# Kernel tuning notes

Hardware: AMD Instinct MI355X
Metric: run time of the kernel (lower is better)

The kernel has to match this reference:

```python
import jax, jax.numpy as jnp
import numpy as np

EMB = 1024
HEADS = 16
DH = EMB // HEADS
EPS = 1e-5


def setup_inputs() -> dict:
    key = jax.random.key(0)
    ks = jax.random.split(key, 8)
    s = 0.02
    return {
        "x": jax.random.normal(ks[0], (4, 2048, EMB), dtype=jnp.float32),
        "Wq": jax.random.normal(ks[1], (EMB, EMB), dtype=jnp.float32) * s,
        "Wk": jax.random.normal(ks[2], (EMB, EMB), dtype=jnp.float32) * s,
        "Wv": jax.random.normal(ks[3], (EMB, EMB), dtype=jnp.float32) * s,
        "Wo": jax.random.normal(ks[4], (EMB, EMB), dtype=jnp.float32) * s,
        "bo": jnp.zeros((EMB,), dtype=jnp.float32),
        "W1": jax.random.normal(ks[5], (EMB, 4 * EMB), dtype=jnp.float32) * s,
        "b1": jnp.zeros((4 * EMB,), dtype=jnp.float32),
        "W2": jax.random.normal(ks[6], (4 * EMB, EMB), dtype=jnp.float32) * s,
        "b2": jnp.zeros((EMB,), dtype=jnp.float32),
        "g1": jnp.ones((EMB,), dtype=jnp.float32),
        "beta1": jnp.zeros((EMB,), dtype=jnp.float32),
        "g2": jnp.ones((EMB,), dtype=jnp.float32),
        "beta2": jnp.zeros((EMB,), dtype=jnp.float32),
    }


def _layernorm(x, scale, bias):
    mean = jnp.mean(x, axis=-1, keepdims=True)
    var = jnp.mean((x - mean) ** 2, axis=-1, keepdims=True)  # unbiased=False
    return scale * ((x - mean) / jnp.sqrt(var + EPS)) + bias


def _attention(x, Wq, Wk, Wv, Wo, bo):
    B, S, _ = x.shape
    q = (x @ Wq).reshape(B, S, HEADS, DH).transpose(0, 2, 1, 3)  # b h s d
    k = (x @ Wk).reshape(B, S, HEADS, DH).transpose(0, 2, 1, 3)
    v = (x @ Wv).reshape(B, S, HEADS, DH).transpose(0, 2, 1, 3)
    scores = jnp.einsum("bhqd,bhkd->bhqk", q, k)
    causal = jnp.tril(jnp.ones((S, S), dtype=bool))
    scores = jnp.where(causal, scores, -jnp.inf)
    w = jax.nn.softmax(scores / jnp.sqrt(jnp.float32(DH)), axis=-1)
    ctx = jnp.einsum("bhqk,bhkd->bhqd", w, v).transpose(0, 2, 1, 3).reshape(B, S, HEADS * DH)
    return ctx @ Wo + bo


def reference(x, Wq, Wk, Wv, Wo, bo, W1, b1, W2, b2, g1, beta1, g2, beta2):
    # pre-LN attention + residual
    h = x + _attention(_layernorm(x, g1, beta1), Wq, Wk, Wv, Wo, bo)
    # pre-LN FFN (exact GELU, as torch nn.GELU default) + residual
    y = _layernorm(h, g2, beta2)
    y = jax.nn.gelu(y @ W1 + b1, approximate=False) @ W2 + b2
    return h + y
```

## Files before the change

### kernel.cpp

```cpp
#include <hip/hip_runtime.h>
#include <hip/hip_bf16.h>

#define EMB 1024
#define SEQ 2048
#define BATCH 4
#define TOK (BATCH*SEQ)
#define NH 16
#define DH 64
#define FF 4096

typedef unsigned short u16;
typedef __bf16 bf16x8 __attribute__((ext_vector_type(8)));
typedef float f32x4 __attribute__((ext_vector_type(4)));

union frag_u { uint4 u4; bf16x8 bf; u16 us[8]; };

__device__ __forceinline__ u16 f2bf(float f) {
  union { float f; unsigned u; } a; a.f = f;
  unsigned r = a.u + 0x7fffu + ((a.u >> 16) & 1u);
  return (u16)(r >> 16);
}
__device__ __forceinline__ float bf2f(u16 u) {
  union { unsigned u; float f; } a; a.u = ((unsigned)u) << 16; return a.f;
}

__device__ __forceinline__ void glds16(const void* g, void* l) {
  __builtin_amdgcn_global_load_lds((const __attribute__((address_space(1))) void*)g,
                                   (__attribute__((address_space(3))) void*)l, 16, 0, 0);
}

__device__ __forceinline__ float gelu_fast(float u) {
  float u2 = u * u;
  float c = fmaf(u2, 0.0356774081f, 0.7978845608f);
  float e = __expf(2.f * u * c);
  return u * e * __builtin_amdgcn_rcpf(e + 1.f);
}

__device__ __forceinline__ void cvt_t_body(const float* __restrict__ src,
                                           u16* __restrict__ dst,
                                           int N, int ldk, int bx, int by) {
  __shared__ float tile[32][33];
  int c0 = bx * 32, r0 = by * 32;
  int tc = threadIdx.x & 31, tr = threadIdx.x >> 5;
  #pragma unroll
  for (int p = 0; p < 4; p++)
    tile[tr + p * 8][tc] = src[(size_t)(r0 + tr + p * 8) * N + c0 + tc];
  __syncthreads();
  #pragma unroll
  for (int p = 0; p < 4; p++)
    dst[(size_t)(c0 + tr + p * 8) * ldk + r0 + tc] = f2bf(tile[tc][tr + p * 8]);
}

__global__ __launch_bounds__(256) void prep_kernel(const float* Wq, const float* Wk,
                                                   const float* Wv, const float* Wo,
                                                   const float* W1, const float* W2,
                                                   u16* wqkv_t, u16* wo_t,
                                                   u16* w1_t, u16* w2_t) {
  int id = blockIdx.x;
  if (id < 4096) {
    const float* s = (id < 1024) ? Wq : (id < 2048) ? Wk : (id < 3072) ? Wv : Wo;
    u16* d = (id < 1024) ? wqkv_t : (id < 2048) ? wqkv_t + 1024 * 1024
           : (id < 3072) ? wqkv_t + 2 * 1024 * 1024 : wo_t;
    int local = id & 1023;
    cvt_t_body(s, d, 1024, 1024, local & 31, local >> 5);
  } else if (id < 8192) {
    int local = id - 4096;
    cvt_t_body(W1, w1_t, 4096, 1024, local & 127, local >> 7);
  } else {
    int local = id - 8192;
    cvt_t_body(W2, w2_t, 1024, 4096, local & 31, local >> 5);
  }
}

template <int IN_BF16>
__global__ __launch_bounds__(256) void ln_kernel(const void* __restrict__ xv,
                                                 const float* __restrict__ g,
                                                 const float* __restrict__ be,
                                                 u16* __restrict__ out) {
  int wave = threadIdx.x >> 6, lane = threadIdx.x & 63;
  int row = blockIdx.x * 4 + wave;
  float v[16];
  float s = 0.f;
  if (IN_BF16) {
    const u16* xr = (const u16*)xv + (size_t)row * EMB;
    #pragma unroll
    for (int i = 0; i < 4; i++) {
      ushort4 u = *(const ushort4*)(xr + i * 256 + lane * 4);
      v[i * 4 + 0] = bf2f(u.x); v[i * 4 + 1] = bf2f(u.y);
      v[i * 4 + 2] = bf2f(u.z); v[i * 4 + 3] = bf2f(u.w);
      s += v[i * 4] + v[i * 4 + 1] + v[i * 4 + 2] + v[i * 4 + 3];
    }
  } else {
    const float* xr = (const float*)xv + (size_t)row * EMB;
    #pragma unroll
    for (int i = 0; i < 4; i++) {
      float4 u = *(const float4*)(xr + i * 256 + lane * 4);
      v[i * 4 + 0] = u.x; v[i * 4 + 1] = u.y; v[i * 4 + 2] = u.z; v[i * 4 + 3] = u.w;
      s += u.x + u.y + u.z + u.w;
    }
  }
  #pragma unroll
  for (int m = 1; m < 64; m <<= 1) s += __shfl_xor(s, m, 64);
  float mean = s * (1.f / EMB);
  float vs = 0.f;
  #pragma unroll
  for (int i = 0; i < 16; i++) { float dx = v[i] - mean; vs += dx * dx; }
  #pragma unroll
  for (int m = 1; m < 64; m <<= 1) vs += __shfl_xor(vs, m, 64);
  float inv = rsqrtf(vs * (1.f / EMB) + 1e-5f);
  u16* orow = out + (size_t)row * EMB;
  #pragma unroll
  for (int i = 0; i < 4; i++) {
    int c = i * 256 + lane * 4;
    float4 gv = *(const float4*)(g + c);
    float4 bv = *(const float4*)(be + c);
    ushort4 o;
    o.x = f2bf(gv.x * (v[i * 4 + 0] - mean) * inv + bv.x);
    o.y = f2bf(gv.y * (v[i * 4 + 1] - mean) * inv + bv.y);
    o.z = f2bf(gv.z * (v[i * 4 + 2] - mean) * inv + bv.z);
    o.w = f2bf(gv.w * (v[i * 4 + 3] - mean) * inv + bv.w);
    *(ushort4*)(orow + c) = o;
  }
}

template <int MODE>
__global__ __launch_bounds__(512) void gemm256(const u16* __restrict__ A,
                                               const u16* __restrict__ Bt,
                                               const float* __restrict__ bias,
                                               void* __restrict__ outp,
                                               int N, int K) {
  __shared__ __align__(16) u16 As[256 * 64];
  __shared__ __align__(16) u16 Bs[128 * 64];
  const int t = threadIdx.x;
  const int w = t >> 6, lane = t & 63;
  const int l15 = lane & 15, quad = lane >> 4;
  const int wr = w >> 1, wc = w & 1;

  const int gx = gridDim.x;
  const int nwg = gx * gridDim.y;
  const int id0 = blockIdx.y * gx + blockIdx.x;
  const int nid = (id0 & 7) * (nwg >> 3) + (id0 >> 3);
  const int rowBase = (nid / gx) * 256, colBase = (nid % gx) * 128;

  const int sr = lane >> 3;
  const int sc = ((lane & 7) ^ sr) * 8;
  const u16* gA = A + (size_t)(rowBase + w * 8 + sr) * K + sc;
  const u16* gB = Bt + (size_t)(colBase + w * 8 + sr) * K + sc;
  u16* lA = As + w * 8 * 64;
  u16* lB = Bs + w * 8 * 64;

  const int swz0 = (quad ^ (l15 & 7)) * 8;
  const int swz1 = ((quad + 4) ^ (l15 & 7)) * 8;

  f32x4 zero = {0.f, 0.f, 0.f, 0.f};
  f32x4 acc[4][4];
  #pragma unroll
  for (int i = 0; i < 4; i++)
    #pragma unroll
    for (int j = 0; j < 4; j++) acc[i][j] = zero;

  for (int k0 = 0; k0 < K; k0 += 64) {
    __syncthreads();
    #pragma unroll
    for (int j = 0; j < 4; j++)
      glds16(gA + (size_t)(j * 64) * K + k0, lA + j * 64 * 64);
    #pragma unroll
    for (int j = 0; j < 2; j++)
      glds16(gB + (size_t)(j * 64) * K + k0, lB + j * 64 * 64);
    __syncthreads();
    #pragma unroll
    for (int kk = 0; kk < 2; kk++) {
      const int so = kk ? swz1 : swz0;
      frag_u a4[4], b4[4];
      #pragma unroll
      for (int mi = 0; mi < 4; mi++)
        a4[mi].u4 = *(const uint4*)(As + (wr * 64 + mi * 16 + l15) * 64 + so);
      #pragma unroll
      for (int ni = 0; ni < 4; ni++)
        b4[ni].u4 = *(const uint4*)(Bs + (wc * 64 + ni * 16 + l15) * 64 + so);
      #pragma unroll
      for (int mi = 0; mi < 4; mi++)
        #pragma unroll
        for (int ni = 0; ni < 4; ni++)
          acc[mi][ni] = __builtin_amdgcn_mfma_f32_16x16x32_bf16(a4[mi].bf, b4[ni].bf, acc[mi][ni], 0, 0, 0);
    }
  }

  #pragma unroll
  for (int mi = 0; mi < 4; mi++) {
    #pragma unroll
    for (int ni = 0; ni < 4; ni++) {
      int col = colBase + wc * 64 + ni * 16 + l15;
      int row0 = rowBase + wr * 64 + mi * 16 + quad * 4;
      if (MODE == 1) {
        int mat = col >> 10, cc = col & 1023;
        int hh = cc >> 6, d = cc & 63;
        int b = row0 >> 11, s0 = row0 & 2047;
        if (mat == 2) {
          uint2 pk;
          pk.x = (unsigned)f2bf(acc[mi][ni][0]) | ((unsigned)f2bf(acc[mi][ni][1]) << 16);
          pk.y = (unsigned)f2bf(acc[mi][ni][2]) | ((unsigned)f2bf(acc[mi][ni][3]) << 16);
          *(uint2*)((u16*)outp + 2 * (size_t)TOK * EMB +
                    ((size_t)((b * NH + hh) * DH + d)) * SEQ + s0) = pk;
        } else {
          #pragma unroll
          for (int r = 0; r < 4; r++)
            ((u16*)outp)[(size_t)mat * (TOK * EMB) +
                         (((size_t)(b * NH + hh) * SEQ + s0 + r) << 6) + d] = f2bf(acc[mi][ni][r]);
        }
      } else {
        #pragma unroll
        for (int r = 0; r < 4; r++) {
          float vv = gelu_fast(acc[mi][ni][r] + bias[col]);
          ((u16*)outp)[(size_t)(row0 + r) * N + col] = f2bf(vv);
        }
      }
    }
  }
}

template <int MODE>
__global__ __launch_bounds__(256) void gemm128(const u16* __restrict__ A,
                                               const u16* __restrict__ Bt,
                                               const float* __restrict__ bias,
                                               const void* __restrict__ resid,
                                               void* __restrict__ outp,
                                               int N, int K) {
  __shared__ __align__(16) u16 As[2][128 * 64];
  __shared__ __align__(16) u16 Bs[2][128 * 64];
  const int t = threadIdx.x;
  const int w = t >> 6, lane = t & 63;
  const int l15 = lane & 15, quad = lane >> 4;
  const int wr = w >> 1, wc = w & 1;

  const int gx = gridDim.x;
  const int nwg = gx * gridDim.y;
  const int id0 = blockIdx.y * gx + blockIdx.x;
  const int nid = (id0 & 7) * (nwg >> 3) + (id0 >> 3);
  const int rowBase = (nid / gx) * 128, colBase = (nid % gx) * 128;

  const int sr = lane >> 3;
  const int sc = ((lane & 7) ^ sr) * 8;
  const u16* gA = A + (size_t)(rowBase + w * 8 + sr) * K + sc;
  const u16* gB = Bt + (size_t)(colBase + w * 8 + sr) * K + sc;
  const int ldsOff = (w * 8) * 64;

  const int swz0 = (quad ^ (l15 & 7)) * 8;
  const int swz1 = ((quad + 4) ^ (l15 & 7)) * 8;

  f32x4 zero = {0.f, 0.f, 0.f, 0.f};
  f32x4 acc[4][4];
  #pragma unroll
  for (int i = 0; i < 4; i++)
    #pragma unroll
    for (int j = 0; j < 4; j++) acc[i][j] = zero;

  const int nt = K >> 6;
  #pragma unroll
  for (int j = 0; j < 4; j++) {
    glds16(gA + (size_t)(j * 32) * K, As[0] + ldsOff + j * 32 * 64);
    glds16(gB + (size_t)(j * 32) * K, Bs[0] + ldsOff + j * 32 * 64);
  }
  __syncthreads();

  for (int tt = 0; tt < nt; tt++) {
    const int cur = tt & 1;
    if (tt + 1 < nt) {
      const int k0 = (tt + 1) << 6;
      #pragma unroll
      for (int j = 0; j < 4; j++) {
        glds16(gA + (size_t)(j * 32) * K + k0, As[cur ^ 1] + ldsOff + j * 32 * 64);
        glds16(gB + (size_t)(j * 32) * K + k0, Bs[cur ^ 1] + ldsOff + j * 32 * 64);
      }
    }
    const u16* as = As[cur];
    const u16* bs = Bs[cur];
    #pragma unroll
    for (int kk = 0; kk < 2; kk++) {
      const int so = kk ? swz1 : swz0;
      frag_u a4[4], b4[4];
      #pragma unroll
      for (int mi = 0; mi < 4; mi++)
        a4[mi].u4 = *(const uint4*)(as + (wr * 64 + mi * 16 + l15) * 64 + so);
      #pragma unroll
      for (int ni = 0; ni < 4; ni++)
        b4[ni].u4 = *(const uint4*)(bs + (wc * 64 + ni * 16 + l15) * 64 + so);
      #pragma unroll
      for (int mi = 0; mi < 4; mi++)
        #pragma unroll
        for (int ni = 0; ni < 4; ni++)
          acc[mi][ni] = __builtin_amdgcn_mfma_f32_16x16x32_bf16(a4[mi].bf, b4[ni].bf, acc[mi][ni], 0, 0, 0);
    }
    __syncthreads();
  }

  #pragma unroll
  for (int mi = 0; mi < 4; mi++) {
    #pragma unroll
    for (int ni = 0; ni < 4; ni++) {
      int col = colBase + wc * 64 + ni * 16 + l15;
      int row0 = rowBase + wr * 64 + mi * 16 + quad * 4;
      #pragma unroll
      for (int r = 0; r < 4; r++) {
        int row = row0 + r;
        float vv = acc[mi][ni][r] + bias[col];
        if (MODE == 3) {
          vv += ((const float*)resid)[(size_t)row * N + col];
          ((u16*)outp)[(size_t)row * N + col] = f2bf(vv);
        } else {
          vv += bf2f(((const u16*)resid)[(size_t)row * N + col]);
          ((float*)outp)[(size_t)row * N + col] = vv;
        }
      }
    }
  }
}

__global__ __launch_bounds__(256) void attn_kernel(const u16* __restrict__ q,
                                                   const u16* __restrict__ k,
                                                   const u16* __restrict__ vt,
                                                   u16* __restrict__ ctx) {
  __shared__ __align__(16) u16 Ks[64 * 72];
  __shared__ __align__(16) u16 Vs[64 * 72];
  __shared__ __align__(16) u16 Ps[128 * 72];
  __shared__ float Ls[128];
  const int t = threadIdx.x;
  const int w = t >> 6, lane = t & 63;
  const int l15 = lane & 15, quad = lane >> 4;
  const int bh = blockIdx.x, pr_ = blockIdx.y;
  const size_t base = (size_t)bh * SEQ * DH;
  const int bq = bh >> 4, hh = bh & 15;

  const int sr = t >> 2, scol = (t & 3) * 8;
  const u16* gK = k + base + (size_t)sr * DH + scol;
  const u16* gV = vt + base + (size_t)sr * SEQ + scol;
  u16* sK = Ks + sr * 72 + scol;
  u16* sV = Vs + sr * 72 + scol;

  f32x4 zero = {0.f, 0.f, 0.f, 0.f};
  uint4 rK0, rK1, rV0, rV1;
  rK0 = *(const uint4*)(gK);
  rK1 = *(const uint4*)(gK + 32);
  rV0 = *(const uint4*)(gV);
  rV1 = *(const uint4*)(gV + 32);

  for (int ti = 0; ti < 2; ti++) {
    const int qt = ti ? (15 - pr_) : pr_;
    const int qBase = qt * 128;
    const int ktEnd = 2 * qt + 1;

    frag_u qf[2][2];
    #pragma unroll
    for (int ni = 0; ni < 2; ni++)
      #pragma unroll
      for (int ks = 0; ks < 2; ks++)
        qf[ni][ks].u4 = *(const uint4*)(q + base +
            (size_t)(qBase + w * 32 + ni * 16 + l15) * DH + ks * 32 + quad * 8);

    f32x4 oacc[2][4];
    #pragma unroll
    for (int mi = 0; mi < 2; mi++)
      #pragma unroll
      for (int n0 = 0; n0 < 4; n0++) oacc[mi][n0] = zero;
    float l0 = 0.f, l1 = 0.f;

    for (int kt = 0; kt <= ktEnd; kt++) {
      __syncthreads();
      *(uint4*)sK = rK0; *(uint4*)(sK + 32) = rK1;
      *(uint4*)sV = rV0; *(uint4*)(sV + 32) = rV1;
      __syncthreads();
      int nkt = (kt < ktEnd) ? kt + 1 : (ti == 0 ? 0 : -1);
      if (nkt >= 0) {
        rK0 = *(const uint4*)(gK + (size_t)(nkt * 64) * DH);
        rK1 = *(const uint4*)(gK + (size_t)(nkt * 64) * DH + 32);
        rV0 = *(const uint4*)(gV + nkt * 64);
        rV1 = *(const uint4*)(gV + nkt * 64 + 32);
      }
      const int rel = kt - 2 * qt;
      if (rel == 1 && w < 2) continue;

      frag_u kf[4][2];
      #pragma unroll
      for (int mi = 0; mi < 4; mi++)
        #pragma unroll
        for (int ks = 0; ks < 2; ks++)
          kf[mi][ks].u4 = *(const uint4*)(Ks + (mi * 16 + l15) * 72 + ks * 32 + quad * 8);
      f32x4 st[4][2];
      #pragma unroll
      for (int mi = 0; mi < 4; mi++)
        #pragma unroll
        for (int ni = 0; ni < 2; ni++) st[mi][ni] = zero;
      #pragma unroll
      for (int ks = 0; ks < 2; ks++)
        #pragma unroll
        for (int mi = 0; mi < 4; mi++)
          #pragma unroll
          for (int ni = 0; ni < 2; ni++)
            st[mi][ni] = __builtin_amdgcn_mfma_f32_16x16x32_bf16(kf[mi][ks].bf, qf[ni][ks].bf, st[mi][ni], 0, 0, 0);

      const bool doMask = (rel == 0 && w < 2) || (rel == 1);
      #pragma unroll
      for (int ni = 0; ni < 2; ni++) {
        const int qrow = qBase + w * 32 + ni * 16 + l15;
        float sum = 0.f;
        u16* prow = Ps + (w * 32 + ni * 16 + l15) * 72;
        #pragma unroll
        for (int mi = 0; mi < 4; mi++) {
          float p[4];
          #pragma unroll
          for (int r = 0; r < 4; r++) {
            p[r] = __expf(st[mi][ni][r] * 0.125f);
            if (doMask && (kt * 64 + mi * 16 + quad * 4 + r) > qrow) p[r] = 0.f;
            sum += p[r];
          }
          uint2 pk;
          pk.x = (unsigned)f2bf(p[0]) | ((unsigned)f2bf(p[1]) << 16);
          pk.y = (unsigned)f2bf(p[2]) | ((unsigned)f2bf(p[3]) << 16);
          *(uint2*)(prow + mi * 16 + quad * 4) = pk;
        }
        sum += __shfl_xor(sum, 16, 64);
        sum += __shfl_xor(sum, 32, 64);
        if (ni == 0) l0 += sum; else l1 += sum;
      }

      frag_u pa[2][2];
      #pragma unroll
      for (int mi = 0; mi < 2; mi++)
        #pragma unroll
        for (int ks = 0; ks < 2; ks++)
          pa[mi][ks].u4 = *(const uint4*)(Ps + (w * 32 + mi * 16 + l15) * 72 + ks * 32 + quad * 8);
      #pragma unroll
      for (int ks = 0; ks < 2; ks++)
        #pragma unroll
        for (int n0 = 0; n0 < 4; n0++) {
          frag_u b;
          b.u4 = *(const uint4*)(Vs + (n0 * 16 + l15) * 72 + ks * 32 + quad * 8);
          #pragma unroll
          for (int mi = 0; mi < 2; mi++)
            oacc[mi][n0] = __builtin_amdgcn_mfma_f32_16x16x32_bf16(pa[mi][ks].bf, b.bf, oacc[mi][n0], 0, 0, 0);
        }
    }

    if (quad == 0) {
      Ls[w * 32 + l15] = l0;
      Ls[w * 32 + 16 + l15] = l1;
    }
    #pragma unroll
    for (int mi = 0; mi < 2; mi++) {
      float il[4];
      #pragma unroll
      for (int r = 0; r < 4; r++) il[r] = 1.f / Ls[w * 32 + mi * 16 + quad * 4 + r];
      #pragma unroll
      for (int n0 = 0; n0 < 4; n0++) {
        int s = qBase + w * 32 + mi * 16 + quad * 4;
        int col = hh * 64 + n0 * 16 + l15;
        #pragma unroll
        for (int r = 0; r < 4; r++)
          ctx[((size_t)(bq * SEQ + s + r)) * EMB + col] = f2bf(oacc[mi][n0][r] * il[r]);
      }
    }
  }
}

extern "C" void kernel_launch(void* const* d_in, const int* in_sizes, int n_in,
                              void* d_out, int out_size, void* d_ws, size_t ws_size,
                              hipStream_t stream) {
  const float* x  = (const float*)d_in[0];
  const float* Wq = (const float*)d_in[1];
  const float* Wk = (const float*)d_in[2];
  const float* Wv = (const float*)d_in[3];
  const float* Wo = (const float*)d_in[4];
  const float* bo = (const float*)d_in[5];
  const float* W1 = (const float*)d_in[6];
  const float* b1 = (const float*)d_in[7];
  const float* W2 = (const float*)d_in[8];
  const float* b2 = (const float*)d_in[9];
  const float* g1  = (const float*)d_in[10];
  const float* be1 = (const float*)d_in[11];
  const float* g2  = (const float*)d_in[12];
  const float* be2 = (const float*)d_in[13];
  float* out = (float*)d_out;
  char* ws = (char*)d_ws;
  const size_t MB = 1u << 20;

  u16* wqkv_t = (u16*)(ws + 0 * MB);
  u16* wo_t   = (u16*)(ws + 6 * MB);
  u16* w1_t   = (u16*)(ws + 8 * MB);
  u16* w2_t   = (u16*)(ws + 16 * MB);
  u16* hbuf   = (u16*)(ws + 24 * MB);
  u16* r1 = (u16*)(ws + 56 * MB);
  u16* qb = (u16*)(ws + 72 * MB);
  u16* f1 = (u16*)(ws + 72 * MB);

  prep_kernel<<<12288, 256, 0, stream>>>(Wq, Wk, Wv, Wo, W1, W2,
                                         wqkv_t, wo_t, w1_t, w2_t);

  ln_kernel<0><<<2048, 256, 0, stream>>>(x, g1, be1, r1);

  gemm256<1><<<dim3(24, 32), 512, 0, stream>>>(r1, wqkv_t, nullptr, qb, 3072, 1024);

  attn_kernel<<<dim3(64, 8), 256, 0, stream>>>(qb, qb + (size_t)TOK * EMB,
                                               qb + 2 * (size_t)TOK * EMB, r1);

  gemm128<3><<<dim3(8, 64), 256, 0, stream>>>(r1, wo_t, bo, x, hbuf, 1024, 1024);

  ln_kernel<1><<<2048, 256, 0, stream>>>(hbuf, g2, be2, r1);

  gemm256<2><<<dim3(32, 32), 512, 0, stream>>>(r1, w1_t, b1, f1, 4096, 1024);

  gemm128<4><<<dim3(8, 64), 256, 0, stream>>>(f1, w2_t, b2, hbuf, out, 1024, 4096);
}
```

Baseline: 461.0 us.

## Split attention into one q-tile per block with swizzled LDS and priority hints

The attention kernel now launches one block per 128-row query tile, 1024 blocks in total, in place of 512 blocks that each processed a paired short and long tile. Heavy tiles are scheduled first by reversing the tile order. The padded LDS layout (stride 72) becomes an unpadded stride-64 layout with XOR swizzling to avoid bank conflicts, and the per-thread load mapping changes to match. It also adds s_setprio around the MFMA sections, a launch bounds occupancy hint, and a separate mask-free exp path for unmasked tiles. The trade-off is more blocks with unequal work, and Q loads and the prefetch chain are no longer shared across the paired tiles.

```diff
diff --git a/kernel.cpp b/kernel.cpp
--- a/kernel.cpp
+++ b/kernel.cpp
@@ -316,148 +316,161 @@
   }
 }
 
-__global__ __launch_bounds__(256) void attn_kernel(const u16* __restrict__ q,
-                                                   const u16* __restrict__ k,
-                                                   const u16* __restrict__ vt,
-                                                   u16* __restrict__ ctx) {
-  __shared__ __align__(16) u16 Ks[64 * 72];
-  __shared__ __align__(16) u16 Vs[64 * 72];
-  __shared__ __align__(16) u16 Ps[128 * 72];
+__global__ __launch_bounds__(256, 4) void attn_kernel(const u16* __restrict__ q,
+                                                      const u16* __restrict__ k,
+                                                      const u16* __restrict__ vt,
+                                                      u16* __restrict__ ctx) {
+  __shared__ __align__(16) u16 Ks[64 * 64];
+  __shared__ __align__(16) u16 Vs[64 * 64];
+  __shared__ __align__(16) u16 Ps[128 * 64];
   __shared__ float Ls[128];
   const int t = threadIdx.x;
   const int w = t >> 6, lane = t & 63;
   const int l15 = lane & 15, quad = lane >> 4;
-  const int bh = blockIdx.x, pr_ = blockIdx.y;
+  const int bh = blockIdx.x;
+  const int qt = 15 - (int)blockIdx.y;
   const size_t base = (size_t)bh * SEQ * DH;
   const int bq = bh >> 4, hh = bh & 15;
-
-  const int sr = t >> 2, scol = (t & 3) * 8;
-  const u16* gK = k + base + (size_t)sr * DH + scol;
-  const u16* gV = vt + base + (size_t)sr * SEQ + scol;
-  u16* sK = Ks + sr * 72 + scol;
-  u16* sV = Vs + sr * 72 + scol;
+  const int qBase = qt * 128;
+  const int ktEnd = 2 * qt + 1;
+  const int l7 = l15 & 7;
+
+  const int r0 = w * 16 + (lane >> 3);
+  const int scg = lane & 7;
+  const int swzs = (scg ^ (r0 & 7)) * 8;
+  const u16* gK = k + base + (size_t)r0 * DH + scg * 8;
+  const u16* gV = vt + base + (size_t)r0 * SEQ + scg * 8;
+  u16* sK0 = Ks + r0 * 64 + swzs;
+  u16* sK1 = Ks + (r0 + 8) * 64 + swzs;
+  u16* sV0 = Vs + r0 * 64 + swzs;
+  u16* sV1 = Vs + (r0 + 8) * 64 + swzs;
+
+  frag_u qf[2][2];
+  #pragma unroll
+  for (int ni = 0; ni < 2; ni++)
+    #pragma unroll
+    for (int ks = 0; ks < 2; ks++)
+      qf[ni][ks].u4 = *(const uint4*)(q + base +
+          (size_t)(qBase + w * 32 + ni * 16 + l15) * DH + ks * 32 + quad * 8);
 
   f32x4 zero = {0.f, 0.f, 0.f, 0.f};
-  uint4 rK0, rK1, rV0, rV1;
-  rK0 = *(const uint4*)(gK);
-  rK1 = *(const uint4*)(gK + 32);
-  rV0 = *(const uint4*)(gV);
-  rV1 = *(const uint4*)(gV + 32);
-
-  for (int ti = 0; ti < 2; ti++) {
-    const int qt = ti ? (15 - pr_) : pr_;
-    const int qBase = qt * 128;
-    const int ktEnd = 2 * qt + 1;
-
-    frag_u qf[2][2];
-    #pragma unroll
-    for (int ni = 0; ni < 2; ni++)
+  f32x4 oacc[2][4];
+  #pragma unroll
+  for (int mi = 0; mi < 2; mi++)
+    #pragma unroll
+    for (int n0 = 0; n0 < 4; n0++) oacc[mi][n0] = zero;
+  float l0 = 0.f, l1 = 0.f;
+
+  uint4 rK0 = *(const uint4*)(gK);
+  uint4 rK1 = *(const uint4*)(gK + 8 * DH);
+  uint4 rV0 = *(const uint4*)(gV);
+  uint4 rV1 = *(const uint4*)(gV + (size_t)8 * SEQ);
+
+  for (int kt = 0; kt <= ktEnd; kt++) {
+    __syncthreads();
+    *(uint4*)sK0 = rK0; *(uint4*)sK1 = rK1;
+    *(uint4*)sV0 = rV0; *(uint4*)sV1 = rV1;
+    __syncthreads();
+    if (kt < ktEnd) {
+      const int no = (kt + 1) * 64;
+      rK0 = *(const uint4*)(gK + (size_t)no * DH);
+      rK1 = *(const uint4*)(gK + (size_t)(no + 8) * DH);
+      rV0 = *(const uint4*)(gV + no);
+      rV1 = *(const uint4*)(gV + (size_t)8 * SEQ + no);
+    }
+    const int rel = kt - 2 * qt;
+    if (rel == 1 && w < 2) continue;
+
+    frag_u kf[4][2];
+    #pragma unroll
+    for (int mi = 0; mi < 4; mi++)
       #pragma unroll
       for (int ks = 0; ks < 2; ks++)
-        qf[ni][ks].u4 = *(const uint4*)(q + base +
-            (size_t)(qBase + w * 32 + ni * 16 + l15) * DH + ks * 32 + quad * 8);
-
-    f32x4 oacc[2][4];
-    #pragma unroll
-    for (int mi = 0; mi < 2; mi++)
-      #pragma unroll
-      for (int n0 = 0; n0 < 4; n0++) oacc[mi][n0] = zero;
-    float l0 = 0.f, l1 = 0.f;
-
-    for (int kt = 0; kt <= ktEnd; kt++) {
-      __syncthreads();
-      *(uint4*)sK = rK0; *(uint4*)(sK + 32) = rK1;
-      *(uint4*)sV = rV0; *(uint4*)(sV + 32) = rV1;
-      __syncthreads();
-      int nkt = (kt < ktEnd) ? kt + 1 : (ti == 0 ? 0 : -1);
-      if (nkt >= 0) {
-        rK0 = *(const uint4*)(gK + (size_t)(nkt * 64) * DH);
-        rK1 = *(const uint4*)(gK + (size_t)(nkt * 64) * DH + 32);
-        rV0 = *(const uint4*)(gV + nkt * 64);
-        rV1 = *(const uint4*)(gV + nkt * 64 + 32);
-      }
-      const int rel = kt - 2 * qt;
-      if (rel == 1 && w < 2) continue;
-
-      frag_u kf[4][2];
+        kf[mi][ks].u4 = *(const uint4*)(Ks + (mi * 16 + l15) * 64 + (((ks * 4 + quad) ^ l7) * 8));
+    f32x4 st[4][2];
+    #pragma unroll
+    for (int mi = 0; mi < 4; mi++)
+      #pragma unroll
+      for (int ni = 0; ni < 2; ni++) st[mi][ni] = zero;
+    __builtin_amdgcn_s_setprio(1);
+    #pragma unroll
+    for (int ks = 0; ks < 2; ks++)
       #pragma unroll
       for (int mi = 0; mi < 4; mi++)
         #pragma unroll
-        for (int ks = 0; ks < 2; ks++)
-          kf[mi][ks].u4 = *(const uint4*)(Ks + (mi * 16 + l15) * 72 + ks * 32 + quad * 8);
-      f32x4 st[4][2];
-      #pragma unroll
-      for (int mi = 0; mi < 4; mi++)
-        #pragma unroll
-        for (int ni = 0; ni < 2; ni++) st[mi][ni] = zero;
-      #pragma unroll
-      for (int ks = 0; ks < 2; ks++)
-        #pragma unroll
-        for (int mi = 0; mi < 4; mi++)
-          #pragma unroll
-          for (int ni = 0; ni < 2; ni++)
-            st[mi][ni] = __builtin_amdgcn_mfma_f32_16x16x32_bf16(kf[mi][ks].bf, qf[ni][ks].bf, st[mi][ni], 0, 0, 0);
-
-      const bool doMask = (rel == 0 && w < 2) || (rel == 1);
-      #pragma unroll
-      for (int ni = 0; ni < 2; ni++) {
-        const int qrow = qBase + w * 32 + ni * 16 + l15;
-        float sum = 0.f;
-        u16* prow = Ps + (w * 32 + ni * 16 + l15) * 72;
-        #pragma unroll
-        for (int mi = 0; mi < 4; mi++) {
-          float p[4];
+        for (int ni = 0; ni < 2; ni++)
+          st[mi][ni] = __builtin_amdgcn_mfma_f32_16x16x32_bf16(kf[mi][ks].bf, qf[ni][ks].bf, st[mi][ni], 0, 0, 0);
+    __builtin_amdgcn_s_setprio(0);
+
+    const bool doMask = (rel == 0 && w < 2) || (rel == 1);
+    #pragma unroll
+    for (int ni = 0; ni < 2; ni++) {
+      const int qrow = qBase + w * 32 + ni * 16 + l15;
+      float sum = 0.f;
+      u16* prow = Ps + (w * 32 + ni * 16 + l15) * 64;
+      #pragma unroll
+      for (int mi = 0; mi < 4; mi++) {
+        float p[4];
+        if (doMask) {
           #pragma unroll
           for (int r = 0; r < 4; r++) {
             p[r] = __expf(st[mi][ni][r] * 0.125f);
-            if (doMask && (kt * 64 + mi * 16 + quad * 4 + r) > qrow) p[r] = 0.f;
+            if ((kt * 64 + mi * 16 + quad * 4 + r) > qrow) p[r] = 0.f;
             sum += p[r];
           }
-          uint2 pk;
-          pk.x = (unsigned)f2bf(p[0]) | ((unsigned)f2bf(p[1]) << 16);
-          pk.y = (unsigned)f2bf(p[2]) | ((unsigned)f2bf(p[3]) << 16);
-          *(uint2*)(prow + mi * 16 + quad * 4) = pk;
+        } else {
+          #pragma unroll
+          for (int r = 0; r < 4; r++) {
+            p[r] = __expf(st[mi][ni][r] * 0.125f);
+            sum += p[r];
+          }
         }
-        sum += __shfl_xor(sum, 16, 64);
-        sum += __shfl_xor(sum, 32, 64);
-        if (ni == 0) l0 += sum; else l1 += sum;
+        uint2 pk;
+        pk.x = (unsigned)f2bf(p[0]) | ((unsigned)f2bf(p[1]) << 16);
+        pk.y = (unsigned)f2bf(p[2]) | ((unsigned)f2bf(p[3]) << 16);
+        *(uint2*)(prow + (((mi * 2 + (quad >> 1)) ^ l7) * 8) + (quad & 1) * 4) = pk;
       }
-
-      frag_u pa[2][2];
-      #pragma unroll
-      for (int mi = 0; mi < 2; mi++)
+      sum += __shfl_xor(sum, 16, 64);
+      sum += __shfl_xor(sum, 32, 64);
+      if (ni == 0) l0 += sum; else l1 += sum;
+    }
+
+    frag_u pa[2][2];
+    #pragma unroll
+    for (int mi = 0; mi < 2; mi++)
+      #pragma unroll
+      for (int ks = 0; ks < 2; ks++)
+        pa[mi][ks].u4 = *(const uint4*)(Ps + (w * 32 + mi * 16 + l15) * 64 + (((ks * 4 + quad) ^ l7) * 8));
+    __builtin_amdgcn_s_setprio(1);
+    #pragma unroll
+    for (int ks = 0; ks < 2; ks++)
+      #pragma unroll
+      for (int n0 = 0; n0 < 4; n0++) {
+        frag_u b;
+        b.u4 = *(const uint4*)(Vs + (n0 * 16 + l15) * 64 + (((ks * 4 + quad) ^ l7) * 8));
         #pragma unroll
-        for (int ks = 0; ks < 2; ks++)
-          pa[mi][ks].u4 = *(const uint4*)(Ps + (w * 32 + mi * 16 + l15) * 72 + ks * 32 + quad * 8);
-      #pragma unroll
-      for (int ks = 0; ks < 2; ks++)
-        #pragma unroll
-        for (int n0 = 0; n0 < 4; n0++) {
-          frag_u b;
-          b.u4 = *(const uint4*)(Vs + (n0 * 16 + l15) * 72 + ks * 32 + quad * 8);
-          #pragma unroll
-          for (int mi = 0; mi < 2; mi++)
-            oacc[mi][n0] = __builtin_amdgcn_mfma_f32_16x16x32_bf16(pa[mi][ks].bf, b.bf, oacc[mi][n0], 0, 0, 0);
-        }
-    }
-
-    if (quad == 0) {
-      Ls[w * 32 + l15] = l0;
-      Ls[w * 32 + 16 + l15] = l1;
-    }
-    #pragma unroll
-    for (int mi = 0; mi < 2; mi++) {
-      float il[4];
-      #pragma unroll
-      for (int r = 0; r < 4; r++) il[r] = 1.f / Ls[w * 32 + mi * 16 + quad * 4 + r];
-      #pragma unroll
-      for (int n0 = 0; n0 < 4; n0++) {
-        int s = qBase + w * 32 + mi * 16 + quad * 4;
-        int col = hh * 64 + n0 * 16 + l15;
-        #pragma unroll
-        for (int r = 0; r < 4; r++)
-          ctx[((size_t)(bq * SEQ + s + r)) * EMB + col] = f2bf(oacc[mi][n0][r] * il[r]);
+        for (int mi = 0; mi < 2; mi++)
+          oacc[mi][n0] = __builtin_amdgcn_mfma_f32_16x16x32_bf16(pa[mi][ks].bf, b.bf, oacc[mi][n0], 0, 0, 0);
       }
+    __builtin_amdgcn_s_setprio(0);
+  }
+
+  if (quad == 0) {
+    Ls[w * 32 + l15] = l0;
+    Ls[w * 32 + 16 + l15] = l1;
+  }
+  #pragma unroll
+  for (int mi = 0; mi < 2; mi++) {
+    float il[4];
+    #pragma unroll
+    for (int r = 0; r < 4; r++) il[r] = 1.f / Ls[w * 32 + mi * 16 + quad * 4 + r];
+    #pragma unroll
+    for (int n0 = 0; n0 < 4; n0++) {
+      int s = qBase + w * 32 + mi * 16 + quad * 4;
+      int col = hh * 64 + n0 * 16 + l15;
+      #pragma unroll
+      for (int r = 0; r < 4; r++)
+        ctx[((size_t)(bq * SEQ + s + r)) * EMB + col] = f2bf(oacc[mi][n0][r] * il[r]);
     }
   }
 }
@@ -499,8 +512,8 @@
 
   gemm256<1><<<dim3(24, 32), 512, 0, stream>>>(r1, wqkv_t, nullptr, qb, 3072, 1024);
 
-  attn_kernel<<<dim3(64, 8), 256, 0, stream>>>(qb, qb + (size_t)TOK * EMB,
-                                               qb + 2 * (size_t)TOK * EMB, r1);
+  attn_kernel<<<dim3(64, 16), 256, 0, stream>>>(qb, qb + (size_t)TOK * EMB,
+                                                qb + 2 * (size_t)TOK * EMB, r1);
 
   gemm128<3><<<dim3(8, 64), 256, 0, stream>>>(r1, wo_t, bo, x, hbuf, 1024, 1024);
 
```

Result: slower. 533.6 us (+15.8%).
